# Kernel tuning notes

Measured on AMD Instinct MI355X. Metric: run time of the kernel, lower is better.

Reference implementation:

```python
import jax, jax.numpy as jnp
import numpy as np

N_HEADS = 16
KV_HEADS = 4
HEAD_DIM = 128
D_MODEL = N_HEADS * HEAD_DIM  # 2048
KV_DIM = KV_HEADS * HEAD_DIM  # 512
MAX_POS = 4096
ROPE_THETA = 10000.0
EPS = 1e-5


def _rope_cache(seq_len):
    # QEffMolmoRotaryEmbedding: inv_freq over head_dim, emb = cat(freqs, freqs)
    inv_freq = 1.0 / (ROPE_THETA ** (jnp.arange(0, HEAD_DIM, 2, dtype=jnp.float32) / HEAD_DIM))
    t = jnp.arange(seq_len, dtype=jnp.float32)
    freqs = jnp.outer(t, inv_freq)                      # [S, D/2]
    emb = jnp.concatenate([freqs, freqs], axis=-1)      # [S, D]
    return jnp.cos(emb), jnp.sin(emb)


def _rotate_half(x):
    # x: [B, H, T, D] -> cat(-x2, x1) with halves along last dim
    x1, x2 = jnp.split(x, 2, axis=-1)
    return jnp.concatenate([-x2, x1], axis=-1)


def _rms_norm(x, w):
    var = jnp.mean(jnp.square(x), axis=-1, keepdims=True)
    return (x * jax.lax.rsqrt(var + EPS)) * w


def setup_inputs() -> dict:
    key = jax.random.key(0)
    ks = jax.random.split(key, 8)
    B, T = 1, 2048
    q = jax.random.normal(ks[0], (B, T, D_MODEL), dtype=jnp.float32)
    k = jax.random.normal(ks[1], (B, T, KV_DIM), dtype=jnp.float32)
    v = jax.random.normal(ks[2], (B, T, KV_DIM), dtype=jnp.float32)
    # causal mask: True means masked (torch.where(mask, -10000, scores))
    attention_mask = jnp.triu(jnp.ones((T, T), dtype=bool), k=1)[None, None]  # [1,1,T,T]
    position_ids = jnp.arange(T, dtype=jnp.int32)[None, :]                    # [B,T]
    q_norm_w = jax.random.normal(ks[3], (D_MODEL,), dtype=jnp.float32) * 0.02 + 1.0
    k_norm_w = jax.random.normal(ks[4], (KV_DIM,), dtype=jnp.float32) * 0.02 + 1.0
    w_out = jax.random.normal(ks[5], (D_MODEL, D_MODEL), dtype=jnp.float32) * (D_MODEL ** -0.5)
    return {"q": q, "k": k, "v": v, "attention_mask": attention_mask,
            "position_ids": position_ids, "q_norm_w": q_norm_w,
            "k_norm_w": k_norm_w, "w_out": w_out}


def reference(q, k, v, attention_mask, position_ids, q_norm_w, k_norm_w, w_out):
    B, T, C = q.shape
    # QK-norm on flat projections
    q = _rms_norm(q, q_norm_w)
    k = _rms_norm(k, k_norm_w)
    # split heads: [B, H, T, D]
    q = q.reshape(B, T, N_HEADS, HEAD_DIM).transpose(0, 2, 1, 3)
    k = k.reshape(B, T, KV_HEADS, HEAD_DIM).transpose(0, 2, 1, 3)
    v = v.reshape(B, T, KV_HEADS, HEAD_DIM).transpose(0, 2, 1, 3)
    # RoPE (rotate_half variant)
    cos_c, sin_c = _rope_cache(MAX_POS)
    cos = cos_c[position_ids][:, None]  # [B,1,T,D]
    sin = sin_c[position_ids][:, None]
    q = q * cos + _rotate_half(q) * sin
    k = k * cos + _rotate_half(k) * sin
    # GQA expand
    rep = N_HEADS // KV_HEADS
    k = jnp.repeat(k, rep, axis=1)
    v = jnp.repeat(v, rep, axis=1)
    scale = 1.0 / np.sqrt(HEAD_DIM)
    scores = jnp.einsum('bhqd,bhkd->bhqk', q, k) * scale  # [B,H,T,T]
    scores = jnp.where(attention_mask, jnp.float32(-10000.0), scores)
    attn = jax.nn.softmax(scores.astype(jnp.float32), axis=-1).astype(q.dtype)
    out = jnp.einsum('bhqk,bhkd->bhqd', attn, v)          # [B,H,T,D]
    out = out.transpose(0, 2, 1, 3).reshape(B, T, C)
    return out @ w_out.T
```

## Files before the change

### kernel.cpp

```cpp
#include <hip/hip_runtime.h>
#include <hip/hip_bf16.h>
#include <math.h>

#define T_SEQ 2048
#define NH 16
#define KVH 4
#define HD 128
#define DM 2048
#define KVD 512

typedef short bf16x8 __attribute__((ext_vector_type(8)));
typedef float f32x4 __attribute__((ext_vector_type(4)));
typedef float f32x16 __attribute__((ext_vector_type(16)));
typedef unsigned int uint2v __attribute__((ext_vector_type(2)));

static __device__ __forceinline__ unsigned short f2bf(float f) {
    unsigned int x = __float_as_uint(f);
    x += 0x7fff + ((x >> 16) & 1);
    return (unsigned short)(x >> 16);
}
static __device__ __forceinline__ float bf2f(unsigned short u) {
    return __uint_as_float(((unsigned int)u) << 16);
}

static __device__ __forceinline__ unsigned int cvtpk(float lo, float hi) {
    unsigned int r;
    asm("v_cvt_pk_bf16_f32 %0, %1, %2" : "=v"(r) : "v"(lo), "v"(hi));
    return r;
}

static __device__ __forceinline__ f32x4 mfma16(bf16x8 a, bf16x8 b, f32x4 c) {
    return __builtin_amdgcn_mfma_f32_16x16x32_bf16(a, b, c, 0, 0, 0);
}
static __device__ __forceinline__ f32x16 mfma32(bf16x8 a, bf16x8 b, f32x16 c) {
    return __builtin_amdgcn_mfma_f32_32x32x16_bf16(a, b, c, 0, 0, 0);
}

static __device__ __forceinline__ void gl_lds16(const unsigned short* g, unsigned short* l) {
    __builtin_amdgcn_global_load_lds(
        (const __attribute__((address_space(1))) unsigned int*)g,
        (__attribute__((address_space(3))) unsigned int*)l,
        16, 0, 0);
}


__global__ __launch_bounds__(256) void prep_all(
    const float* __restrict__ q, const float* __restrict__ k,
    const float* __restrict__ qw, const float* __restrict__ kw,
    const int* __restrict__ pos_ids,
    unsigned short* __restrict__ Qb, unsigned short* __restrict__ Ks,
    const float* __restrict__ v, unsigned short* __restrict__ Vs,
    const float* __restrict__ w, unsigned short* __restrict__ Wf) {
    int bid = blockIdx.x;
    int tid = threadIdx.x;
    __shared__ float smem[DM + KVD + 64 + 64 + 8];

    if (bid < 2048) {
        float* qr = smem;
        float* kr = smem + DM;
        float* cosL = smem + DM + KVD;
        float* sinL = cosL + 64;
        float* redq = sinL + 64;
        float* redk = redq + 4;
        int t = bid;
        float qs = 0.f, ks = 0.f;
        {
            const float* qp = q + (size_t)t * DM + tid * 8;
            float4 v0 = *(const float4*)(qp);
            float4 v1 = *(const float4*)(qp + 4);
            float* dst = qr + tid * 8;
            dst[0] = v0.x; dst[1] = v0.y; dst[2] = v0.z; dst[3] = v0.w;
            dst[4] = v1.x; dst[5] = v1.y; dst[6] = v1.z; dst[7] = v1.w;
            qs = v0.x * v0.x + v0.y * v0.y + v0.z * v0.z + v0.w * v0.w +
                 v1.x * v1.x + v1.y * v1.y + v1.z * v1.z + v1.w * v1.w;
            float2 kv = *(const float2*)(k + (size_t)t * KVD + tid * 2);
            kr[tid * 2] = kv.x; kr[tid * 2 + 1] = kv.y;
            ks = kv.x * kv.x + kv.y * kv.y;
        }
        if (tid < 64) {
            float pos = (float)pos_ids[t];
            float inv = powf(10000.0f, -(float)tid * (1.0f / 64.0f));
            float a = pos * inv;
            cosL[tid] = cosf(a);
            sinL[tid] = sinf(a);
        }
        for (int off = 32; off; off >>= 1) {
            qs += __shfl_down(qs, off);
            ks += __shfl_down(ks, off);
        }
        if ((tid & 63) == 0) { redq[tid >> 6] = qs; redk[tid >> 6] = ks; }
        __syncthreads();
        float qinv = rsqrtf((redq[0] + redq[1] + redq[2] + redq[3]) * (1.0f / DM) + 1e-5f);
        float kinv = rsqrtf((redk[0] + redk[1] + redk[2] + redk[3]) * (1.0f / KVD) + 1e-5f);
        {
            int base = tid * 8;
            int h = base >> 7;
            int d = base & 127;
            bool lo = d < 64;
            int i0 = d & 63;
            int pb = lo ? base + 64 : base - 64;
            #pragma unroll
            for (int j = 0; j < 8; ++j) {
                float xv = qr[base + j] * qinv * qw[base + j];
                float pv = qr[pb + j] * qinv * qw[pb + j];
                float c = cosL[i0 + j];
                float s = sinL[i0 + j];
                float o = lo ? (xv * c - pv * s) : (xv * c + pv * s);
                Qb[((size_t)h * T_SEQ + t) * HD + d + j] = f2bf(o);
            }
        }
        {
            int base = tid * 2;
            int kh = base >> 7;
            int d = base & 127;
            bool lo = d < 64;
            int i0 = d & 63;
            int pb = lo ? base + 64 : base - 64;
            int kt = t >> 5, lq = t & 31;
            #pragma unroll
            for (int j = 0; j < 2; ++j) {
                float xv = kr[base + j] * kinv * kw[base + j];
                float pv = kr[pb + j] * kinv * kw[pb + j];
                float c = cosL[i0 + j];
                float s = sinL[i0 + j];
                float o = lo ? (xv * c - pv * s) : (xv * c + pv * s);
                int dj = d + j;
                int sl = dj >> 4, hi2 = (dj >> 3) & 1, jj = dj & 7;
                size_t oi = ((((size_t)(kh * 64 + kt) * 8 + sl) * 2 + hi2) * 32 + lq) * 8 + jj;
                Ks[oi] = f2bf(o);
            }
        }
        return;
    }
    if (bid < 2304) {
        unsigned short* tile = (unsigned short*)smem;
        int vb = bid - 2048;
        int tb = vb & 31;
        int cb = vb >> 5;
        #pragma unroll 4
        for (int rep = 0; rep < 16; ++rep) {
            int e = rep * 256 + tid;
            int r = e >> 6;
            int c = e & 63;
            tile[c * 80 + r] = f2bf(v[(size_t)(tb * 64 + r) * KVD + cb * 64 + c]);
        }
        __syncthreads();
        #pragma unroll
        for (int rep = 0; rep < 2; ++rep) {
            int e = rep * 256 + tid;
            int cc = e >> 3, tg = e & 7;
            int cg = cb * 64 + cc;
            int kh = cg >> 7, crow = cg & 127, db = crow >> 5, lq = crow & 31;
            int t0g = tb * 64 + tg * 8;
            int kt = t0g >> 5, tr = t0g & 31, half = tr >> 4, hi2 = (tr >> 3) & 1;
            size_t o = (((((size_t)(kh * 64 + kt) * 2 + half) * 4 + db) * 2 + hi2) * 32 + lq) * 8;
            *(bf16x8*)(Vs + o) = *(const bf16x8*)(&tile[cc * 80 + tg * 8]);
        }
        return;
    }
    {
        size_t idx = ((size_t)(bid - 2304) * 256 + tid) * 4;
        int row = (int)(idx >> 11);
        int col = (int)(idx & 2047);
        float4 f = *(const float4*)(w + idx);
        ushort4 o;
        o.x = f2bf(f.x); o.y = f2bf(f.y); o.z = f2bf(f.z); o.w = f2bf(f.w);
        int nt = row >> 6, wn2 = (row >> 5) & 1, jb = (row >> 4) & 1, lr = row & 15;
        int kt = col >> 6, ks = (col >> 5) & 1, hi2 = (col >> 3) & 3, jj = col & 7;
        size_t off = (((size_t)(nt * 32 + kt) * 8) + (wn2 * 2 + jb) * 2 + ks) * 512
                   + (lr + 16 * hi2) * 8 + jj;
        *(ushort4*)(Wf + off) = o;
    }
}

#define BEXP 20.0f
#define SCALE2 (0.08838834764831845f * 1.4426950408889634f)

#define STAGE1(B, S, KT)                                                           \
    do {                                                                           \
        const unsigned short* kg_ = Kt_g + (size_t)(KT) * 4096;                    \
        const unsigned short* vg_ = Vt_g + (size_t)(KT) * 4096;                    \
        gl_lds16(kg_ + w * 512 + l * 8,        &kv[B][S][w * 512]);                \
        gl_lds16(kg_ + 2048 + w * 512 + l * 8, &kv[B][S][2048 + w * 512]);         \
        gl_lds16(vg_ + w * 512 + l * 8,        &kv[B][S][4096 + w * 512]);         \
        gl_lds16(vg_ + 2048 + w * 512 + l * 8, &kv[B][S][6144 + w * 512]);         \
    } while (0)

#define TILE_COMPUTE(BUF, SLOT, KT)                                                \
    do {                                                                           \
        const unsigned short* kl = &kv[BUF][SLOT][0] + l * 8;                      \
        const unsigned short* vl = &kv[BUF][SLOT][4096] + l * 8;                   \
        f32x16 sa, sb;                                                             \
        _Pragma("unroll") for (int r = 0; r < 16; ++r) { sa[r] = 0.f; sb[r] = 0.f; } \
        __builtin_amdgcn_s_setprio(1);                                             \
        _Pragma("unroll") for (int x = 0; x < 8; x += 2) {                         \
            bf16x8 k0 = *(const bf16x8*)(kl + x * 512);                            \
            bf16x8 k1 = *(const bf16x8*)(kl + (x + 1) * 512);                      \
            sa = mfma32(k0, qf[x], sa);                                            \
            sb = mfma32(k1, qf[x + 1], sb);                                        \
        }                                                                          \
        __builtin_amdgcn_s_setprio(0);                                             \
        float p_[16];                                                              \
        if ((KT) == nkt - 1) {                                                     \
            int lim = qglob - (KT) * 32;                                           \
            _Pragma("unroll") for (int r = 0; r < 16; ++r) {                       \
                float e_ = __builtin_amdgcn_exp2f((sa[r] + sb[r]) * SCALE2 - BEXP); \
                int off_ = (r & 3) + 8 * (r >> 2) + 4 * hi;                        \
                p_[r] = (off_ <= lim) ? e_ : 0.f;                                  \
                sden4[r & 3] += p_[r];                                             \
            }                                                                      \
        } else {                                                                   \
            _Pragma("unroll") for (int r = 0; r < 16; ++r) {                       \
                p_[r] = __builtin_amdgcn_exp2f((sa[r] + sb[r]) * SCALE2 - BEXP);   \
                sden4[r & 3] += p_[r];                                             \
            }                                                                      \
        }                                                                          \
        __builtin_amdgcn_s_setprio(1);                                             \
        _Pragma("unroll") for (int half = 0; half < 2; ++half) {                   \
            unsigned int a0 = cvtpk(p_[half * 8 + 0], p_[half * 8 + 1]);           \
            unsigned int a1 = cvtpk(p_[half * 8 + 2], p_[half * 8 + 3]);           \
            unsigned int b0 = cvtpk(p_[half * 8 + 4], p_[half * 8 + 5]);           \
            unsigned int b1 = cvtpk(p_[half * 8 + 6], p_[half * 8 + 7]);           \
            uint2v w0 = __builtin_amdgcn_permlane32_swap(a0, b0, false, false);    \
            uint2v w1 = __builtin_amdgcn_permlane32_swap(a1, b1, false, false);    \
            union { unsigned int u[4]; bf16x8 v; } pc;                             \
            pc.u[0] = w0[0]; pc.u[1] = w1[0]; pc.u[2] = w0[1]; pc.u[3] = w1[1];    \
            bf16x8 pf = pc.v;                                                      \
            _Pragma("unroll") for (int db = 0; db < 4; ++db) {                     \
                bf16x8 vf = *(const bf16x8*)(vl + (half * 4 + db) * 512);          \
                oacc[db] = mfma32(vf, pf, oacc[db]);                               \
            }                                                                      \
        }                                                                          \
        __builtin_amdgcn_s_setprio(0);                                             \
    } while (0)

__global__ __launch_bounds__(256) void attn_fwd22(
    const unsigned short* __restrict__ Qb, const unsigned short* __restrict__ Ks,
    const unsigned short* __restrict__ Vs,
    unsigned short* __restrict__ Opart, float* __restrict__ Lpart,
    unsigned short* __restrict__ Xf, int CHUNK) {
    int fid = blockIdx.x;
    int sid = fid >> 2;
    int kh = fid & 3;
    int qrow, seg;
    if (sid < 60)       { qrow = 63 - sid / 3;          seg = sid % 3; }
    else if (sid < 104) { int t2 = sid - 60; qrow = 43 - (t2 >> 1); seg = t2 & 1; }
    else                { qrow = 21 - (sid - 104);      seg = 0; }

    int tid = threadIdx.x;
    int w = tid >> 6, l = tid & 63;
    int h = kh * 4 + w;
    int lq = l & 31, hi = l >> 5;
    int qglob = qrow * 32 + lq;

    int nkt = qrow + 1;
    int t0 = seg * CHUNK;
    int t1 = min(t0 + CHUNK, nkt);
    size_t idx = (size_t)(h * 64 + qrow) * 4 + seg;

    const unsigned short* Qh = Qb + (size_t)h * T_SEQ * HD;
    const unsigned short* Kt_g = Ks + (size_t)kh * 64 * 4096;
    const unsigned short* Vt_g = Vs + (size_t)kh * 64 * 4096;

    __shared__ unsigned short kv[2][2][8192];

    bf16x8 qf[8];
    #pragma unroll
    for (int sl = 0; sl < 8; ++sl)
        qf[sl] = *(const bf16x8*)(Qh + (size_t)qglob * HD + sl * 16 + hi * 8);

    f32x16 oacc[4];
    #pragma unroll
    for (int db = 0; db < 4; ++db)
        #pragma unroll
        for (int r = 0; r < 16; ++r) oacc[db][r] = 0.f;
    f32x4 sden4 = (f32x4){0.f, 0.f, 0.f, 0.f};

    int pairsEnd = t0 + ((t1 - t0) & ~1);
    int kt = t0;
    int cur = 0;
    if (kt < pairsEnd) { STAGE1(0, 0, kt); STAGE1(0, 1, kt + 1); }
    if (kt + 2 < pairsEnd) { STAGE1(1, 0, kt + 2); STAGE1(1, 1, kt + 3); }
    for (; kt < pairsEnd; kt += 2) {
        bool more = (kt + 2 < pairsEnd);
        if (more) asm volatile("s_waitcnt vmcnt(8)" ::: "memory");
        else      asm volatile("s_waitcnt vmcnt(0)" ::: "memory");
        __builtin_amdgcn_s_barrier();
        TILE_COMPUTE(cur, 0, kt);
        TILE_COMPUTE(cur, 1, kt + 1);
        asm volatile("s_waitcnt lgkmcnt(0)" ::: "memory");
        __builtin_amdgcn_s_barrier();
        if (kt + 4 < pairsEnd) { STAGE1(cur, 0, kt + 4); STAGE1(cur, 1, kt + 5); }
        cur ^= 1;
    }
    if (kt < t1) {
        STAGE1(cur, 0, kt);
        asm volatile("s_waitcnt vmcnt(0)" ::: "memory");
        __builtin_amdgcn_s_barrier();
        TILE_COMPUTE(cur, 0, kt);
    }

    float sden = (sden4[0] + sden4[1]) + (sden4[2] + sden4[3]);
    float sden_tot = sden + __shfl_xor(sden, 32);

    if (t0 == 0 && t1 == nkt) {
        float invs = 1.0f / sden_tot;
        int mt = qglob >> 7, wmrow = (qglob >> 6) & 1, ii = (qglob >> 4) & 3, lr = qglob & 15;
        size_t baseA = (((size_t)mt * 32) * 16 + (wmrow * 4 + ii) * 2) * 512 + lr * 8;
        #pragma unroll
        for (int db = 0; db < 4; ++db) {
            size_t bdb = baseA + (size_t)(h * 2 + (db >> 1)) * 8192 + (size_t)(db & 1) * 512;
            #pragma unroll
            for (int r = 0; r < 16; ++r) {
                size_t off = bdb + (r >> 2) * 128 + (r & 3) + 4 * hi;
                Xf[off] = f2bf(oacc[db][r] * invs);
            }
        }
        return;
    }
    if (hi == 0) Lpart[idx * 32 + lq] = sden_tot;
    unsigned short* op = Opart + (idx << 12);
    #pragma unroll
    for (int db = 0; db < 4; ++db) {
        #pragma unroll
        for (int r = 0; r < 16; ++r) {
            int d = db * 32 + (r & 3) + 8 * (r >> 2) + 4 * hi;
            op[d * 32 + lq] = f2bf(oacc[db][r]);
        }
    }
}

__global__ __launch_bounds__(256) void attn_combine(
    const unsigned short* __restrict__ Opart, const float* __restrict__ Lpart,
    unsigned short* __restrict__ Xf, int CHUNK) {
    int qrow = CHUNK + blockIdx.x;
    int h = blockIdx.y;
    int tid = threadIdx.x;
    int nkt = qrow + 1;
    int used = (nkt + CHUNK - 1) / CHUNK;
    int base = (h * 64 + qrow) * 4;
    __shared__ float invden[32];
    if (tid < 32) {
        int q = tid;
        float den = 0.f;
        for (int s = 0; s < used; ++s) den += Lpart[(base + s) * 32 + q];
        invden[q] = 1.0f / den;
    }
    __syncthreads();
    int d = tid >> 1, q0 = (tid & 1) * 16;
    float acc[16];
    #pragma unroll
    for (int j = 0; j < 16; ++j) acc[j] = 0.f;
    for (int s = 0; s < used; ++s) {
        const unsigned short* op = Opart + ((size_t)(base + s) << 12) + d * 32 + q0;
        bf16x8 o0 = *(const bf16x8*)(op);
        bf16x8 o1 = *(const bf16x8*)(op + 8);
        #pragma unroll
        for (int j = 0; j < 8; ++j) {
            acc[j]     += bf2f((unsigned short)o0[j]);
            acc[8 + j] += bf2f((unsigned short)o1[j]);
        }
    }
    __shared__ unsigned short xo[32][136];
    #pragma unroll
    for (int j = 0; j < 16; ++j)
        xo[q0 + j][d] = f2bf(acc[j] * invden[q0 + j]);
    __syncthreads();
    int q = tid >> 3, dc = (tid & 7) * 16;
    bf16x8 v0 = *(const bf16x8*)(&xo[q][dc]);
    bf16x8 v1 = *(const bf16x8*)(&xo[q][dc + 8]);
    int row = qrow * 32 + q;
    int mt = row >> 7, wmrow = (row >> 6) & 1, ii = (row >> 4) & 3, lr = row & 15;
    int kt = h * 2 + (dc >> 6);
    int ks = (dc >> 5) & 1;
    int hi2 = (dc >> 3) & 3;
    size_t off = (((size_t)(mt * 32 + kt) * 16) + (wmrow * 4 + ii) * 2 + ks) * 512
               + (lr + 16 * hi2) * 8;
    *(bf16x8*)(Xf + off) = v0;
    *(bf16x8*)(Xf + off + 128) = v1;
}

__global__ __launch_bounds__(256) void outproj5(
    const unsigned short* __restrict__ Xf, const unsigned short* __restrict__ Wf,
    float* __restrict__ out) {
    __shared__ unsigned short Af[3][8192];
    __shared__ unsigned short Bf[3][4096];
    int tid = threadIdx.x;
    int w = tid >> 6, l = tid & 63;
    int lr = l & 15, lg = l >> 4;
    int wm = w >> 1, wn = w & 1;
    int id = blockIdx.x;
    int wg = (id & 7) * 64 + (id >> 3);
    int s = wg >> 5, wi = wg & 31;
    int mb = (s & 3) * 4 + (wi & 3);
    int nb = (s >> 2) * 8 + (wi >> 2);
    int m0 = mb * 128, n0 = nb * 64;

    const unsigned short* Xt = Xf + ((size_t)mb * 32 * 16) * 512 + l * 8;
    const unsigned short* Wt = Wf + ((size_t)nb * 32 * 8) * 512 + l * 8;

    f32x4 acc[4][2];
    #pragma unroll
    for (int i = 0; i < 4; ++i)
        #pragma unroll
        for (int j = 0; j < 2; ++j) acc[i][j] = (f32x4){0.f, 0.f, 0.f, 0.f};

#define OSTAGE(B, KT)                                                              \
    do {                                                                           \
        const unsigned short* xa = Xt + (size_t)(KT) * 8192;                       \
        const unsigned short* wb_ = Wt + (size_t)(KT) * 4096;                      \
        unsigned short* afb = &Af[B][0];                                           \
        unsigned short* bfb = &Bf[B][0];                                           \
        _Pragma("unroll") for (int u = 0; u < 4; ++u)                              \
            gl_lds16(xa + (w * 4 + u) * 512, afb + (w * 4 + u) * 512);             \
        _Pragma("unroll") for (int u = 0; u < 2; ++u)                              \
            gl_lds16(wb_ + (w * 2 + u) * 512, bfb + (w * 2 + u) * 512);            \
    } while (0)

    OSTAGE(0, 0);
    OSTAGE(1, 1);
    OSTAGE(2, 2);
    int cur = 0;
    for (int t = 0; t < 32; ++t) {
        if (t <= 29)      asm volatile("s_waitcnt vmcnt(12)" ::: "memory");
        else if (t == 30) asm volatile("s_waitcnt vmcnt(6)" ::: "memory");
        else              asm volatile("s_waitcnt vmcnt(0)" ::: "memory");
        __builtin_amdgcn_s_barrier();
        __builtin_amdgcn_s_setprio(1);
        #pragma unroll
        for (int ks = 0; ks < 2; ++ks) {
            bf16x8 af[4], bfr[2];
            #pragma unroll
            for (int i = 0; i < 4; ++i)
                af[i] = *(const bf16x8*)(&Af[cur][((wm * 4 + i) * 2 + ks) * 512] + l * 8);
            #pragma unroll
            for (int j = 0; j < 2; ++j)
                bfr[j] = *(const bf16x8*)(&Bf[cur][((wn * 2 + j) * 2 + ks) * 512] + l * 8);
            #pragma unroll
            for (int i = 0; i < 4; ++i)
                #pragma unroll
                for (int j = 0; j < 2; ++j)
                    acc[i][j] = mfma16(af[i], bfr[j], acc[i][j]);
        }
        __builtin_amdgcn_s_setprio(0);
        asm volatile("s_waitcnt lgkmcnt(0)" ::: "memory");
        __builtin_amdgcn_s_barrier();
        if (t + 3 < 32) OSTAGE(cur, t + 3);
        cur = (cur == 2) ? 0 : cur + 1;
    }
    #pragma unroll
    for (int i = 0; i < 4; ++i) {
        #pragma unroll
        for (int j = 0; j < 2; ++j) {
            #pragma unroll
            for (int r = 0; r < 4; ++r) {
                int row = m0 + wm * 64 + i * 16 + lg * 4 + r;
                int col = n0 + wn * 32 + j * 16 + lr;
                out[(size_t)row * DM + col] = acc[i][j][r];
            }
        }
    }
}

extern "C" void kernel_launch(void* const* d_in, const int* in_sizes, int n_in,
                              void* d_out, int out_size, void* d_ws, size_t ws_size,
                              hipStream_t stream) {
    const float* q = (const float*)d_in[0];
    const float* k = (const float*)d_in[1];
    const float* v = (const float*)d_in[2];
    const int* pos_ids = (const int*)d_in[4];
    const float* qw = (const float*)d_in[5];
    const float* kw = (const float*)d_in[6];
    const float* wout = (const float*)d_in[7];
    float* out = (float*)d_out;

    char* ws = (char*)d_ws;
    unsigned short* Qb = (unsigned short*)(ws + 0x100000);
    unsigned short* Ks = (unsigned short*)(ws + 0x900000);
    unsigned short* Vs = (unsigned short*)(ws + 0xB00000);
    unsigned short* Wf = (unsigned short*)(ws + 0xD00000);
    unsigned short* Xf = (unsigned short*)(ws + 0x1500000);
    float* Lpart = (float*)(ws + 0x1D00000);
    unsigned short* Opart = (unsigned short*)(ws + 0x1E00000);

    int CHUNK = (ws_size >= 0x1E00000ull + 4ull * 0x800000ull) ? 22 : 64;

    prep_all<<<2048 + 256 + 4096, 256, 0, stream>>>(q, k, qw, kw, pos_ids, Qb, Ks,
                                                    v, Vs, wout, Wf);
    if (CHUNK == 22) {
        attn_fwd22<<<504, 256, 0, stream>>>(Qb, Ks, Vs, Opart, Lpart, Xf, CHUNK);
        attn_combine<<<dim3(64 - 22, NH), 256, 0, stream>>>(Opart, Lpart, Xf, CHUNK);
    } else {
        attn_fwd22<<<504, 256, 0, stream>>>(Qb, Ks, Vs, Opart, Lpart, Xf, 64);
    }
    outproj5<<<512, 256, 0, stream>>>(Xf, Wf, out);
}
```

Measured before the change: 84.63 us.

## Process two query row-tiles per wave to reuse K/V LDS fragments

Each wave now handles a pair of adjacent 32-row query tiles, so every K and V fragment read from LDS feeds two MFMAs instead of one. The goal is to halve K/V LDS traffic and global staging per unit of work, and to halve the grid size. The split-KV schedule is remapped to query-row pairs, and the causal mask now covers the last two tiles. In exchange, register pressure roughly doubles (two Q fragment sets, two output accumulators), which may lower occupancy. With fewer, larger blocks load balance may also suffer.

```diff
diff --git a/kernel.cpp b/kernel.cpp
--- a/kernel.cpp
+++ b/kernel.cpp
@@ -186,55 +186,66 @@
         gl_lds16(vg_ + 2048 + w * 512 + l * 8, &kv[B][S][6144 + w * 512]);         \
     } while (0)
 
-#define TILE_COMPUTE(BUF, SLOT, KT)                                                \
+#define PACKP(P, PF)                                                               \
+    unsigned int PF##a0 = cvtpk(P[half * 8 + 0], P[half * 8 + 1]);                 \
+    unsigned int PF##a1 = cvtpk(P[half * 8 + 2], P[half * 8 + 3]);                 \
+    unsigned int PF##b0 = cvtpk(P[half * 8 + 4], P[half * 8 + 5]);                 \
+    unsigned int PF##b1 = cvtpk(P[half * 8 + 6], P[half * 8 + 7]);                 \
+    uint2v PF##w0 = __builtin_amdgcn_permlane32_swap(PF##a0, PF##b0, false, false);\
+    uint2v PF##w1 = __builtin_amdgcn_permlane32_swap(PF##a1, PF##b1, false, false);\
+    union { unsigned int u[4]; bf16x8 v; } PF##pc;                                 \
+    PF##pc.u[0] = PF##w0[0]; PF##pc.u[1] = PF##w1[0];                              \
+    PF##pc.u[2] = PF##w0[1]; PF##pc.u[3] = PF##w1[1];                              \
+    bf16x8 PF = PF##pc.v;
+
+#define TILE_COMPUTE2(BUF, SLOT, KT)                                               \
     do {                                                                           \
         const unsigned short* kl = &kv[BUF][SLOT][0] + l * 8;                      \
         const unsigned short* vl = &kv[BUF][SLOT][4096] + l * 8;                   \
-        f32x16 sa, sb;                                                             \
-        _Pragma("unroll") for (int r = 0; r < 16; ++r) { sa[r] = 0.f; sb[r] = 0.f; } \
+        f32x16 sA, sB;                                                             \
+        _Pragma("unroll") for (int r = 0; r < 16; ++r) { sA[r] = 0.f; sB[r] = 0.f; } \
         __builtin_amdgcn_s_setprio(1);                                             \
-        _Pragma("unroll") for (int x = 0; x < 8; x += 2) {                         \
-            bf16x8 k0 = *(const bf16x8*)(kl + x * 512);                            \
-            bf16x8 k1 = *(const bf16x8*)(kl + (x + 1) * 512);                      \
-            sa = mfma32(k0, qf[x], sa);                                            \
-            sb = mfma32(k1, qf[x + 1], sb);                                        \
+        _Pragma("unroll") for (int x = 0; x < 8; ++x) {                            \
+            bf16x8 kf = *(const bf16x8*)(kl + x * 512);           \
+            sA = mfma32(kf, qfA[x], sA);                                           \
+            sB = mfma32(kf, qfB[x], sB);                                           \
         }                                                                          \
         __builtin_amdgcn_s_setprio(0);                                             \
-        float p_[16];                                                              \
-        if ((KT) == nkt - 1) {                                                     \
-            int lim = qglob - (KT) * 32;                                           \
+        float pA[16], pB[16];                                                      \
+        if ((KT) >= nkt - 2) {                                                     \
+            int limA = qgA - (KT) * 32;                                            \
+            int limB = qgB - (KT) * 32;                                            \
             _Pragma("unroll") for (int r = 0; r < 16; ++r) {                       \
-                float e_ = __builtin_amdgcn_exp2f((sa[r] + sb[r]) * SCALE2 - BEXP); \
                 int off_ = (r & 3) + 8 * (r >> 2) + 4 * hi;                        \
-                p_[r] = (off_ <= lim) ? e_ : 0.f;                                  \
-                sden4[r & 3] += p_[r];                                             \
+                float eA = __builtin_amdgcn_exp2f(sA[r] * SCALE2 - BEXP);          \
+                float eB = __builtin_amdgcn_exp2f(sB[r] * SCALE2 - BEXP);          \
+                pA[r] = (off_ <= limA) ? eA : 0.f;                                 \
+                pB[r] = (off_ <= limB) ? eB : 0.f;                                 \
+                sdA4[r & 3] += pA[r];                                              \
+                sdB4[r & 3] += pB[r];                                              \
             }                                                                      \
         } else {                                                                   \
             _Pragma("unroll") for (int r = 0; r < 16; ++r) {                       \
-                p_[r] = __builtin_amdgcn_exp2f((sa[r] + sb[r]) * SCALE2 - BEXP);   \
-                sden4[r & 3] += p_[r];                                             \
+                pA[r] = __builtin_amdgcn_exp2f(sA[r] * SCALE2 - BEXP);             \
+                pB[r] = __builtin_amdgcn_exp2f(sB[r] * SCALE2 - BEXP);             \
+                sdA4[r & 3] += pA[r];                                              \
+                sdB4[r & 3] += pB[r];                                              \
             }                                                                      \
         }                                                                          \
         __builtin_amdgcn_s_setprio(1);                                             \
         _Pragma("unroll") for (int half = 0; half < 2; ++half) {                   \
-            unsigned int a0 = cvtpk(p_[half * 8 + 0], p_[half * 8 + 1]);           \
-            unsigned int a1 = cvtpk(p_[half * 8 + 2], p_[half * 8 + 3]);           \
-            unsigned int b0 = cvtpk(p_[half * 8 + 4], p_[half * 8 + 5]);           \
-            unsigned int b1 = cvtpk(p_[half * 8 + 6], p_[half * 8 + 7]);           \
-            uint2v w0 = __builtin_amdgcn_permlane32_swap(a0, b0, false, false);    \
-            uint2v w1 = __builtin_amdgcn_permlane32_swap(a1, b1, false, false);    \
-            union { unsigned int u[4]; bf16x8 v; } pc;                             \
-            pc.u[0] = w0[0]; pc.u[1] = w1[0]; pc.u[2] = w0[1]; pc.u[3] = w1[1];    \
-            bf16x8 pf = pc.v;                                                      \
+            PACKP(pA, pfA)                                                         \
+            PACKP(pB, pfB)                                                         \
             _Pragma("unroll") for (int db = 0; db < 4; ++db) {                     \
-                bf16x8 vf = *(const bf16x8*)(vl + (half * 4 + db) * 512);          \
-                oacc[db] = mfma32(vf, pf, oacc[db]);                               \
+                bf16x8 vf = *(const bf16x8*)(vl + (half * 4 + db) * 512);  \
+                oA[db] = mfma32(vf, pfA, oA[db]);                                  \
+                oB[db] = mfma32(vf, pfB, oB[db]);                                  \
             }                                                                      \
         }                                                                          \
         __builtin_amdgcn_s_setprio(0);                                             \
     } while (0)
 
-__global__ __launch_bounds__(256) void attn_fwd22(
+__global__ __launch_bounds__(256) void attn_fwd25(
     const unsigned short* __restrict__ Qb, const unsigned short* __restrict__ Ks,
     const unsigned short* __restrict__ Vs,
     unsigned short* __restrict__ Opart, float* __restrict__ Lpart,
@@ -242,21 +253,27 @@
     int fid = blockIdx.x;
     int sid = fid >> 2;
     int kh = fid & 3;
-    int qrow, seg;
-    if (sid < 60)       { qrow = 63 - sid / 3;          seg = sid % 3; }
-    else if (sid < 104) { int t2 = sid - 60; qrow = 43 - (t2 >> 1); seg = t2 & 1; }
-    else                { qrow = 21 - (sid - 104);      seg = 0; }
+    int qpair, seg;
+    if (CHUNK == 22) {
+        if (sid < 30)      { qpair = 31 - sid / 3;               seg = sid % 3; }
+        else if (sid < 52) { int t2 = sid - 30; qpair = 21 - (t2 >> 1); seg = t2 & 1; }
+        else               { qpair = 10 - (sid - 52);            seg = 0; }
+    } else {
+        qpair = 31 - sid;  seg = 0;
+    }
 
     int tid = threadIdx.x;
     int w = tid >> 6, l = tid & 63;
     int h = kh * 4 + w;
     int lq = l & 31, hi = l >> 5;
-    int qglob = qrow * 32 + lq;
-
-    int nkt = qrow + 1;
+    int qrowA = qpair * 2, qrowB = qrowA + 1;
+    int qgA = qrowA * 32 + lq;
+    int qgB = qrowB * 32 + lq;
+
+    int nkt = qpair * 2 + 2;
     int t0 = seg * CHUNK;
     int t1 = min(t0 + CHUNK, nkt);
-    size_t idx = (size_t)(h * 64 + qrow) * 4 + seg;
+    if (t0 >= t1) return;
 
     const unsigned short* Qh = Qb + (size_t)h * T_SEQ * HD;
     const unsigned short* Kt_g = Ks + (size_t)kh * 64 * 4096;
@@ -264,17 +281,20 @@
 
     __shared__ unsigned short kv[2][2][8192];
 
-    bf16x8 qf[8];
-    #pragma unroll
-    for (int sl = 0; sl < 8; ++sl)
-        qf[sl] = *(const bf16x8*)(Qh + (size_t)qglob * HD + sl * 16 + hi * 8);
-
-    f32x16 oacc[4];
+    bf16x8 qfA[8], qfB[8];
+    #pragma unroll
+    for (int sl = 0; sl < 8; ++sl) {
+        qfA[sl] = *(const bf16x8*)(Qh + (size_t)qgA * HD + sl * 16 + hi * 8);
+        qfB[sl] = *(const bf16x8*)(Qh + (size_t)qgB * HD + sl * 16 + hi * 8);
+    }
+
+    f32x16 oA[4], oB[4];
     #pragma unroll
     for (int db = 0; db < 4; ++db)
         #pragma unroll
-        for (int r = 0; r < 16; ++r) oacc[db][r] = 0.f;
-    f32x4 sden4 = (f32x4){0.f, 0.f, 0.f, 0.f};
+        for (int r = 0; r < 16; ++r) { oA[db][r] = 0.f; oB[db][r] = 0.f; }
+    f32x4 sdA4 = (f32x4){0.f, 0.f, 0.f, 0.f};
+    f32x4 sdB4 = (f32x4){0.f, 0.f, 0.f, 0.f};
 
     int pairsEnd = t0 + ((t1 - t0) & ~1);
     int kt = t0;
@@ -286,8 +306,8 @@
         if (more) asm volatile("s_waitcnt vmcnt(8)" ::: "memory");
         else      asm volatile("s_waitcnt vmcnt(0)" ::: "memory");
         __builtin_amdgcn_s_barrier();
-        TILE_COMPUTE(cur, 0, kt);
-        TILE_COMPUTE(cur, 1, kt + 1);
+        TILE_COMPUTE2(cur, 0, kt);
+        TILE_COMPUTE2(cur, 1, kt + 1);
         asm volatile("s_waitcnt lgkmcnt(0)" ::: "memory");
         __builtin_amdgcn_s_barrier();
         if (kt + 4 < pairsEnd) { STAGE1(cur, 0, kt + 4); STAGE1(cur, 1, kt + 5); }
@@ -297,35 +317,59 @@
         STAGE1(cur, 0, kt);
         asm volatile("s_waitcnt vmcnt(0)" ::: "memory");
         __builtin_amdgcn_s_barrier();
-        TILE_COMPUTE(cur, 0, kt);
-    }
-
-    float sden = (sden4[0] + sden4[1]) + (sden4[2] + sden4[3]);
-    float sden_tot = sden + __shfl_xor(sden, 32);
+        TILE_COMPUTE2(cur, 0, kt);
+    }
+
+    float sA = (sdA4[0] + sdA4[1]) + (sdA4[2] + sdA4[3]);
+    float sB = (sdB4[0] + sdB4[1]) + (sdB4[2] + sdB4[3]);
+    float sAt = sA + __shfl_xor(sA, 32);
+    float sBt = sB + __shfl_xor(sB, 32);
 
     if (t0 == 0 && t1 == nkt) {
-        float invs = 1.0f / sden_tot;
-        int mt = qglob >> 7, wmrow = (qglob >> 6) & 1, ii = (qglob >> 4) & 3, lr = qglob & 15;
-        size_t baseA = (((size_t)mt * 32) * 16 + (wmrow * 4 + ii) * 2) * 512 + lr * 8;
-        #pragma unroll
-        for (int db = 0; db < 4; ++db) {
-            size_t bdb = baseA + (size_t)(h * 2 + (db >> 1)) * 8192 + (size_t)(db & 1) * 512;
-            #pragma unroll
-            for (int r = 0; r < 16; ++r) {
-                size_t off = bdb + (r >> 2) * 128 + (r & 3) + 4 * hi;
-                Xf[off] = f2bf(oacc[db][r] * invs);
+        float iA = 1.0f / sAt, iB = 1.0f / sBt;
+        {
+            int mt = qgA >> 7, wmrow = (qgA >> 6) & 1, ii = (qgA >> 4) & 3, lr = qgA & 15;
+            size_t baseA = (((size_t)mt * 32) * 16 + (wmrow * 4 + ii) * 2) * 512 + lr * 8;
+            #pragma unroll
+            for (int db = 0; db < 4; ++db) {
+                size_t bdb = baseA + (size_t)(h * 2 + (db >> 1)) * 8192 + (size_t)(db & 1) * 512;
+                #pragma unroll
+                for (int r = 0; r < 16; ++r) {
+                    size_t off = bdb + (r >> 2) * 128 + (r & 3) + 4 * hi;
+                    Xf[off] = f2bf(oA[db][r] * iA);
+                }
             }
         }
+        {
+            int mt = qgB >> 7, wmrow = (qgB >> 6) & 1, ii = (qgB >> 4) & 3, lr = qgB & 15;
+            size_t baseB = (((size_t)mt * 32) * 16 + (wmrow * 4 + ii) * 2) * 512 + lr * 8;
+            #pragma unroll
+            for (int db = 0; db < 4; ++db) {
+                size_t bdb = baseB + (size_t)(h * 2 + (db >> 1)) * 8192 + (size_t)(db & 1) * 512;
+                #pragma unroll
+                for (int r = 0; r < 16; ++r) {
+                    size_t off = bdb + (r >> 2) * 128 + (r & 3) + 4 * hi;
+                    Xf[off] = f2bf(oB[db][r] * iB);
+                }
+            }
+        }
         return;
     }
-    if (hi == 0) Lpart[idx * 32 + lq] = sden_tot;
-    unsigned short* op = Opart + (idx << 12);
+    size_t idxA = (size_t)(h * 64 + qrowA) * 4 + seg;
+    size_t idxB = (size_t)(h * 64 + qrowB) * 4 + seg;
+    if (hi == 0) {
+        Lpart[idxA * 32 + lq] = sAt;
+        Lpart[idxB * 32 + lq] = sBt;
+    }
+    unsigned short* opA = Opart + (idxA << 12);
+    unsigned short* opB = Opart + (idxB << 12);
     #pragma unroll
     for (int db = 0; db < 4; ++db) {
         #pragma unroll
         for (int r = 0; r < 16; ++r) {
             int d = db * 32 + (r & 3) + 8 * (r >> 2) + 4 * hi;
-            op[d * 32 + lq] = f2bf(oacc[db][r]);
+            opA[d * 32 + lq] = f2bf(oA[db][r]);
+            opB[d * 32 + lq] = f2bf(oB[db][r]);
         }
     }
 }
@@ -488,10 +532,10 @@
     prep_all<<<2048 + 256 + 4096, 256, 0, stream>>>(q, k, qw, kw, pos_ids, Qb, Ks,
                                                     v, Vs, wout, Wf);
     if (CHUNK == 22) {
-        attn_fwd22<<<504, 256, 0, stream>>>(Qb, Ks, Vs, Opart, Lpart, Xf, CHUNK);
+        attn_fwd25<<<252, 256, 0, stream>>>(Qb, Ks, Vs, Opart, Lpart, Xf, CHUNK);
         attn_combine<<<dim3(64 - 22, NH), 256, 0, stream>>>(Opart, Lpart, Xf, CHUNK);
     } else {
-        attn_fwd22<<<504, 256, 0, stream>>>(Qb, Ks, Vs, Opart, Lpart, Xf, 64);
+        attn_fwd25<<<128, 256, 0, stream>>>(Qb, Ks, Vs, Opart, Lpart, Xf, 64);
     }
     outproj5<<<512, 256, 0, stream>>>(Xf, Wf, out);
 }
```

Result: no change. 86.30 us (+2.0%).
